# Kernel optimization log

Hardware: AMD Instinct MI355X
Metric: run time of the kernel (lower is better)

Reference implementation:

```python
import jax, jax.numpy as jnp
import numpy as np

B, LC, LT = 2, 1024, 1024
DS, DF = 2, 1
EOBS = 4                 # nn.Embed(2, 4)
D_IN = EOBS + DS + DF    # concat(obs, s, f)
EMB_H, D = 256, 64       # embed_obs_s_f = MLP([256, 64])
H, DH = 8, 8             # heads x head_dim = D
FFN_H = 128              # ffn = MLP([128, 64])
BIAS_H = 16              # DistanceBias hidden width
HEAD_H = 128             # head = MLP([128, 2])
NBLK = 6                 # num_blks (num_reps = 1)
EPS = 1e-6

def _ln(x, scale, bias):
    mu = jnp.mean(x, -1, keepdims=True)
    var = jnp.var(x, -1, keepdims=True)
    return (x - mu) * jax.lax.rsqrt(var + EPS) * scale + bias

def _mlp(x, w1, b1, w2, b2):
    return jax.nn.relu(x @ w1 + b1) @ w2 + b2

def _dist_bias(d, w1, b1, w2, b2):
    # d: [B, Lq, Lk] scalar distances -> per-head bias [B, H, Lq, Lk]
    h = jax.nn.relu(d[..., None] @ w1 + b1)
    return jnp.transpose(h @ w2 + b2, (0, 3, 1, 2))

def _mha(q_in, kv_in, wq, bq, wk, bk, wv, bv, wo, bo, bias):
    q = (q_in @ wq + bq).reshape(*q_in.shape[:-1], H, DH)
    k = (kv_in @ wk + bk).reshape(*kv_in.shape[:-1], H, DH)
    v = (kv_in @ wv + bv).reshape(*kv_in.shape[:-1], H, DH)
    scores = jnp.einsum('bqhd,bkhd->bhqk', q, k) / np.sqrt(DH).astype(np.float32) + bias
    a = jax.nn.softmax(scores, axis=-1)
    o = jnp.einsum('bhqk,bkhd->bqhd', a, v).reshape(*q_in.shape[:-1], D)
    return o @ wo + bo

def _forward(s_ctx, f_ctx, s_test, embed_obs_table, emb_w1, emb_b1, emb_w2, emb_b2,
             attn_wq, attn_bq, attn_wk, attn_bk, attn_wv, attn_bv, attn_wo, attn_bo,
             ffn_w1, ffn_b1, ffn_w2, ffn_b2, bias_w1, bias_b1, bias_w2, bias_b2,
             norm_scale, norm_bias, fnorm_scale, fnorm_bias,
             head_w1, head_b1, head_w2, head_b2):
    Bv, Lt = s_test.shape[0], s_test.shape[1]
    f_test = jnp.zeros((Bv, Lt, f_ctx.shape[-1]), f_ctx.dtype)
    obs = jnp.broadcast_to(embed_obs_table[1], (*f_ctx.shape[:-1], EOBS))
    unobs = jnp.broadcast_to(embed_obs_table[0], (Bv, Lt, EOBS))
    kvs = _mlp(jnp.concatenate([obs, s_ctx, f_ctx], -1), emb_w1, emb_b1, emb_w2, emb_b2)
    qvs = _mlp(jnp.concatenate([unobs, s_test, f_test], -1), emb_w1, emb_b1, emb_w2, emb_b2)
    # vmap(l2_dist_sq): pairwise squared L2 distances per batch element
    d_qk = jnp.sum((s_test[:, :, None, :] - s_ctx[:, None, :, :]) ** 2, -1)
    d_kk = jnp.sum((s_ctx[:, :, None, :] - s_ctx[:, None, :, :]) ** 2, -1)
    for i in range(NBLK):
        b_qk = _dist_bias(d_qk, bias_w1[i], bias_b1[i], bias_w2[i], bias_b2[i])
        b_kk = _dist_bias(d_kk, bias_w1[i], bias_b1[i], bias_w2[i], bias_b2[i])
        aw = (attn_wq[i], attn_bq[i], attn_wk[i], attn_bk[i], attn_wv[i], attn_bv[i], attn_wo[i], attn_bo[i])
        ns, nb = norm_scale[i], norm_bias[i]
        q_att = _ln(qvs + _mha(qvs, kvs, *aw, b_qk), ns, nb)
        k_att = _ln(kvs + _mha(kvs, kvs, *aw, b_kk), ns, nb)
        qvs = _ln(q_att + _mlp(q_att, ffn_w1[i], ffn_b1[i], ffn_w2[i], ffn_b2[i]), ns, nb)
        kvs = _ln(k_att + _mlp(k_att, ffn_w1[i], ffn_b1[i], ffn_w2[i], ffn_b2[i]), ns, nb)
    qvs = _ln(qvs, fnorm_scale, fnorm_bias)
    f_dist = _mlp(qvs, head_w1, head_b1, head_w2, head_b2)
    f_mu, f_log_var = jnp.split(f_dist, 2, axis=-1)
    f_std = jnp.exp(f_log_var / 2)  # min_std = 0.0
    return f_mu, f_std

def setup_inputs() -> dict:
    key = jax.random.key(0)
    ks = iter(jax.random.split(key, 40))
    r = lambda shp, s=0.05: jax.random.normal(next(ks), shp, jnp.float32) * s
    return dict(
        s_ctx=r((B, LC, DS), 1.0), f_ctx=r((B, LC, DF), 1.0), s_test=r((B, LT, DS), 1.0),
        embed_obs_table=r((2, EOBS)),
        emb_w1=r((D_IN, EMB_H)), emb_b1=jnp.zeros((EMB_H,)),
        emb_w2=r((EMB_H, D)), emb_b2=jnp.zeros((D,)),
        attn_wq=r((NBLK, D, D)), attn_bq=jnp.zeros((NBLK, D)),
        attn_wk=r((NBLK, D, D)), attn_bk=jnp.zeros((NBLK, D)),
        attn_wv=r((NBLK, D, D)), attn_bv=jnp.zeros((NBLK, D)),
        attn_wo=r((NBLK, D, D)), attn_bo=jnp.zeros((NBLK, D)),
        ffn_w1=r((NBLK, D, FFN_H)), ffn_b1=jnp.zeros((NBLK, FFN_H)),
        ffn_w2=r((NBLK, FFN_H, D)), ffn_b2=jnp.zeros((NBLK, D)),
        bias_w1=r((NBLK, 1, BIAS_H)), bias_b1=jnp.zeros((NBLK, BIAS_H)),
        bias_w2=r((NBLK, BIAS_H, H)), bias_b2=jnp.zeros((NBLK, H)),
        norm_scale=jnp.ones((NBLK, D)), norm_bias=jnp.zeros((NBLK, D)),
        fnorm_scale=jnp.ones((D,)), fnorm_bias=jnp.zeros((D,)),
        head_w1=r((D, HEAD_H)), head_b1=jnp.zeros((HEAD_H,)),
        head_w2=r((HEAD_H, 2)), head_b2=jnp.zeros((2,)),
    )

def reference(s_ctx, f_ctx, s_test, embed_obs_table, emb_w1, emb_b1, emb_w2, emb_b2,
              attn_wq, attn_bq, attn_wk, attn_bk, attn_wv, attn_bv, attn_wo, attn_bo,
              ffn_w1, ffn_b1, ffn_w2, ffn_b2, bias_w1, bias_b1, bias_w2, bias_b2,
              norm_scale, norm_bias, fnorm_scale, fnorm_bias,
              head_w1, head_b1, head_w2, head_b2):
    return _forward(s_ctx, f_ctx, s_test, embed_obs_table, emb_w1, emb_b1, emb_w2, emb_b2,
                    attn_wq, attn_bq, attn_wk, attn_bk, attn_wv, attn_bv, attn_wo, attn_bo,
                    ffn_w1, ffn_b1, ffn_w2, ffn_b2, bias_w1, bias_b1, bias_w2, bias_b2,
                    norm_scale, norm_bias, fnorm_scale, fnorm_bias,
                    head_w1, head_b1, head_w2, head_b2)
```

## Files before the change

### kernel.cpp

```cpp
#include <hip/hip_runtime.h>
#include <hip/hip_bf16.h>

typedef __hip_bfloat16 bf16;
typedef float v2f __attribute__((ext_vector_type(2)));

#define LEN 1024
#define N2 2048
#define SCALE_L2E 0.5100697918f

#define I_SCTX   0
#define I_FCTX   4096
#define I_STEST  6144
#define I_OBS    10240
#define I_EW1    10248
#define I_EB1    12040
#define I_EW2    12296
#define I_EB2    28680
#define I_WQ     28744
#define I_BQ     53320
#define I_WK     53704
#define I_BK     78280
#define I_WV     78664
#define I_BV     103240
#define I_WO     103624
#define I_BO     128200
#define I_FW1    128584
#define I_FB1    177736
#define I_FW2    178504
#define I_FB2    227656
#define I_BW1    228040
#define I_BB1    228136
#define I_BW2    228232
#define I_BB2    229000
#define I_NS     229048
#define I_NB     229432
#define I_FNS    229816
#define I_FNB    229880
#define I_HW1    229944
#define I_HB1    238136
#define I_HW2    238264
#define I_HB2    238520

#define OFF_FLAG 240000
#define OFF_PW   240256
#define OFF_QVS  262144
#define OFF_KVS  393216
#define OFF_Q1   524288
#define OFF_Q2   655360
#define OFF_KB   786432
#define OFF_VB   917504
#define OFF_PART 1048576

__constant__ int C_OFFS[33] = {
    0, 4096, 6144, 10240, 10248, 12040, 12296, 28680, 28744, 53320, 53704,
    78280, 78664, 103240, 103624, 128200, 128584, 177736, 178504, 227656,
    228040, 228136, 228232, 229000, 229048, 229432, 229816, 229880, 229944,
    238136, 238264, 238520, 238522 };

struct InPtrs { const void* p[32]; };

__global__ void k_flag(const void* ns_raw, float* ws) {
    if (threadIdx.x == 0) {
        unsigned u = *(const unsigned*)ns_raw;
        ((int*)(ws + OFF_FLAG))[0] = (u == 0x3F803F80u) ? 1 : 0;
    }
}

__global__ __launch_bounds__(256) void k_cvt(InPtrs ptrs, float* ws) {
    __shared__ int sflag;
    if (threadIdx.x == 0) sflag = ((const int*)(ws + OFF_FLAG))[0];
    __syncthreads();
    const int isbf = sflag;
    const int i = blockIdx.y;
    const int o0 = C_OFFS[i], n = C_OFFS[i + 1] - o0;
    const void* src = ptrs.p[i];
    for (int j = blockIdx.x * 256 + threadIdx.x; j < n; j += gridDim.x * 256) {
        float v = isbf ? __bfloat162float(((const bf16*)src)[j])
                       : ((const float*)src)[j];
        ws[o0 + j] = v;
    }
}

__global__ __launch_bounds__(256) void k_pw(float* ws) {
    const int L = blockIdx.x, t = threadIdx.x;
    __shared__ float w1s[16], b1s[16], bps[16];
    __shared__ int rnk[16];
    if (t < 16) {
        float w = ws[I_BW1 + L * 16 + t], b0 = ws[I_BB1 + L * 16 + t];
        w1s[t] = w; b1s[t] = b0;
        bps[t] = (w != 0.f) ? (-b0 / w) : 1e30f;
    }
    __syncthreads();
    if (t < 16) {
        float me = bps[t]; int r = 0;
        for (int j = 0; j < 16; ++j) {
            float o = bps[j];
            if (o < me || (o == me && j < t)) ++r;
        }
        rnk[t] = r;
    }
    __syncthreads();
    if (t < 16) ws[OFF_PW + L * 288 + 272 + rnk[t]] = bps[t];
    if (t < 136) {
        int s = t >> 3, h = t & 7;
        float slope = 0.f, inter = ws[I_BB2 + L * 8 + h];
        for (int j = 0; j < 16; ++j) {
            float w = w1s[j];
            bool act = (w > 0.f) ? (rnk[j] < s)
                     : (w < 0.f) ? (rnk[j] >= s)
                                 : (b1s[j] > 0.f);
            if (act) {
                float w2v = ws[I_BW2 + L * 128 + j * 8 + h];
                slope += w * w2v;
                inter += b1s[j] * w2v;
            }
        }
        const float LOG2E = 1.4426950408889634f;
        ws[OFF_PW + L * 288 + (s * 8 + h) * 2]     = slope * LOG2E;
        ws[OFF_PW + L * 288 + (s * 8 + h) * 2 + 1] = inter * LOG2E;
    }
}

__global__ __launch_bounds__(256) void k_embed(float* ws) {
    __shared__ float hbuf[256];
    __shared__ float red[256];
    int r = blockIdx.x, t = threadIdx.x;
    bool is_ctx = (r < N2);
    int rr = is_ctx ? r : r - N2;
    const float* ob = ws + I_OBS + (is_ctx ? 4 : 0);
    const float* s  = ws + (is_ctx ? I_SCTX : I_STEST);
    float in[7];
    in[0] = ob[0]; in[1] = ob[1]; in[2] = ob[2]; in[3] = ob[3];
    in[4] = s[rr * 2]; in[5] = s[rr * 2 + 1];
    in[6] = is_ctx ? ws[I_FCTX + rr] : 0.f;

    float acc = ws[I_EB1 + t];
#pragma unroll
    for (int i = 0; i < 7; ++i) acc += in[i] * ws[I_EW1 + i * 256 + t];
    hbuf[t] = fmaxf(acc, 0.f);
    __syncthreads();

    int d = t & 63, p = t >> 6;
    float a2 = 0.f;
#pragma unroll 8
    for (int j = p * 64; j < p * 64 + 64; ++j) a2 += hbuf[j] * ws[I_EW2 + j * 64 + d];
    red[t] = a2;
    __syncthreads();
    if (t < 64) {
        float o = red[t] + red[64 + t] + red[128 + t] + red[192 + t] + ws[I_EB2 + t];
        float* dst = ws + (is_ctx ? OFF_KVS : OFF_QVS);
        dst[rr * 64 + t] = o;
    }
}

__global__ __launch_bounds__(256) void k_qkv(int blk, float* ws) {
    __shared__ float xs[2][64];
    int r = blockIdx.x, t = threadIdx.x;
    if (t < 64)       xs[0][t] = ws[OFF_QVS + r * 64 + t];
    else if (t < 128) xs[1][t - 64] = ws[OFF_KVS + r * 64 + (t - 64)];
    __syncthreads();
    int o = t >> 6, d = t & 63;
    const float* x = (o == 0) ? xs[0] : xs[1];
    const float* W; const float* bb; float* dst;
    if (o <= 1)      { W = ws + I_WQ + blk * 4096; bb = ws + I_BQ + blk * 64; dst = ws + (o == 0 ? OFF_Q1 : OFF_Q2); }
    else if (o == 2) { W = ws + I_WK + blk * 4096; bb = ws + I_BK + blk * 64; dst = ws + OFF_KB; }
    else             { W = ws + I_WV + blk * 4096; bb = ws + I_BV + blk * 64; dst = ws + OFF_VB; }
    float acc = bb[d];
#pragma unroll 8
    for (int k = 0; k < 64; ++k) acc += x[k] * W[k * 64 + d];
    dst[r * 64 + d] = acc;
}

__global__ __launch_bounds__(256, 5) void k_attn(int blk, float* ws) {
    __shared__ float Ks[2176];
    __shared__ float Vs[2176];
    __shared__ v2f   Sds[544];
    __shared__ v2f   pw[136];

    const int t = threadIdx.x;
    const int qt = blockIdx.x, ks = blockIdx.y, z = blockIdx.z;
    const int b = z & 1, kind = z >> 1;
    const int q0 = qt * 16;
    const float* Qbuf = ws + (kind == 0 ? OFF_Q1 : OFF_Q2);
    const float* Kbuf = ws + OFF_KB;
    const float* Vbuf = ws + OFF_VB;
    const float* sq_src = ws + (kind == 0 ? I_STEST : I_SCTX);
    const float* sk_src = ws + I_SCTX;
    const float* pwg = ws + OFF_PW + blk * 288;

    float bp[16];
#pragma unroll
    for (int j = 0; j < 16; ++j) bp[j] = pwg[272 + j];

    if (t < 136) pw[t] = (v2f){ pwg[t * 2], pwg[t * 2 + 1] };

    const int q2 = t >> 4, h2 = (t >> 1) & 7, par = t & 1;
    const int tk = t & 15;

    v2f qf[4];
    {
        const float* qp = Qbuf + (b * LEN + q0 + q2) * 64 + h2 * 8;
        float4 qa = *(const float4*)qp;
        float4 qb = *(const float4*)(qp + 4);
        qf[0] = (v2f){qa.x, qa.y}; qf[1] = (v2f){qa.z, qa.w};
        qf[2] = (v2f){qb.x, qb.y}; qf[3] = (v2f){qb.z, qb.w};
    }
    float sqx, sqy;
    {
        const float* sp = sq_src + (b * LEN + q0 + q2) * 2;
        sqx = sp[0]; sqy = sp[1];
    }

    float m = -1e30f, lsum = 0.f;
    v2f oacc[4] = {};

    for (int kt = ks * 8; kt < ks * 8 + 8; ++kt) {
        __syncthreads();
        {
            int kr = t >> 3, j = (t & 7) * 8;
            const float* ksrc = Kbuf + (b * LEN + kt * 32 + kr) * 64 + j;
            const float* vsrc = Vbuf + (b * LEN + kt * 32 + kr) * 64 + j;
            *(float4*)&Ks[kr * 68 + j]     = *(const float4*)ksrc;
            *(float4*)&Ks[kr * 68 + j + 4] = *(const float4*)(ksrc + 4);
            *(float4*)&Vs[kr * 68 + j]     = *(const float4*)vsrc;
            *(float4*)&Vs[kr * 68 + j + 4] = *(const float4*)(vsrc + 4);
        }
        {
            float4 kc = *(const float4*)(sk_src + (b * LEN + kt * 32 + tk * 2) * 2);
            float dx0 = sqx - kc.x, dy0 = sqy - kc.y;
            float dx1 = sqx - kc.z, dy1 = sqy - kc.w;
            float d0 = dx0 * dx0 + dy0 * dy0;
            float d1 = dx1 * dx1 + dy1 * dy1;
            int s0 = 0, s1 = 0;
#pragma unroll
            for (int j = 0; j < 16; ++j) { s0 += (d0 > bp[j]); s1 += (d1 > bp[j]); }
            Sds[(tk * 2) * 17 + q2]     = (v2f){d0, (float)s0};
            Sds[(tk * 2 + 1) * 17 + q2] = (v2f){d1, (float)s1};
        }
        __syncthreads();

        float sv[16];
#pragma unroll
        for (int j = 0; j < 16; ++j) {
            int k = par + 2 * j;
            v2f dsv = Sds[k * 17 + q2];
            v2f pv_ = pw[(int)dsv.y * 8 + h2];
            const v2f* kf = (const v2f*)&Ks[k * 68 + h2 * 8];
            v2f acc = qf[0] * kf[0];
            acc += qf[1] * kf[1];
            acc += qf[2] * kf[2];
            acc += qf[3] * kf[3];
            sv[j] = (acc.x + acc.y) * SCALE_L2E + (pv_.x * dsv.x + pv_.y);
        }
        float tm = m;
#pragma unroll
        for (int j = 0; j < 16; ++j) tm = fmaxf(tm, sv[j]);
        float alpha = exp2f(m - tm);
        lsum *= alpha;
        v2f av = (v2f){alpha, alpha};
#pragma unroll
        for (int c = 0; c < 4; ++c) oacc[c] *= av;
#pragma unroll
        for (int j = 0; j < 16; ++j) {
            int k = par + 2 * j;
            float p = exp2f(sv[j] - tm);
            lsum += p;
            const v2f* vf = (const v2f*)&Vs[k * 68 + h2 * 8];
            v2f pp = (v2f){p, p};
            oacc[0] += pp * vf[0];
            oacc[1] += pp * vf[1];
            oacc[2] += pp * vf[2];
            oacc[3] += pp * vf[3];
        }
        m = tm;
    }

    {
        float mo = __shfl_xor(m, 1);
        float Mx = fmaxf(m, mo);
        float a0 = exp2f(m - Mx), a1 = exp2f(mo - Mx);
        float lo = __shfl_xor(lsum, 1);
        float Lt = lsum * a0 + lo * a1;
        float ov[8];
#pragma unroll
        for (int c = 0; c < 4; ++c) {
            v2f x = oacc[c];
            ov[2 * c]     = x.x * a0 + __shfl_xor(x.x, 1) * a1;
            ov[2 * c + 1] = x.y * a0 + __shfl_xor(x.y, 1) * a1;
        }
        if (par == 0) {
            float* p = ws + OFF_PART + (z * LEN + q0 + q2) * 384 + (h2 * 4 + ks) * 12;
            *(float4*)(p)     = make_float4(ov[0], ov[1], ov[2], ov[3]);
            *(float4*)(p + 4) = make_float4(ov[4], ov[5], ov[6], ov[7]);
            *(float4*)(p + 8) = make_float4(Mx, Lt, 0.f, 0.f);
        }
    }
}

__global__ __launch_bounds__(128) void k_fuse(int blk, float* ws) {
    __shared__ float raw[384];
    __shared__ float xo[64];
    __shared__ float xs[64];
    __shared__ float hs[128];
    __shared__ float xn[64];
    const int r = blockIdx.x, kind = blockIdx.y, t = threadIdx.x;
    const int b = r >> 10, row = r & 1023;
    const int z = kind * 2 + b;
    float* io = ws + (kind == 0 ? OFF_QVS : OFF_KVS);

    const float* pbase = ws + OFF_PART + (z * LEN + row) * 384;
    if (t < 96) *(float4*)&raw[t * 4] = *(const float4*)&pbase[t * 4];
    __syncthreads();

    if (t < 64) {
        int h = t >> 3, d = t & 7;
        float M = -1e30f;
#pragma unroll
        for (int k2 = 0; k2 < 4; ++k2) M = fmaxf(M, raw[(h * 4 + k2) * 12 + 8]);
        float L = 0.f, o = 0.f;
#pragma unroll
        for (int k2 = 0; k2 < 4; ++k2) {
            float e = exp2f(raw[(h * 4 + k2) * 12 + 8] - M);
            L += raw[(h * 4 + k2) * 12 + 9] * e;
            o += raw[(h * 4 + k2) * 12 + d] * e;
        }
        xo[t] = o / L;
    }
    __syncthreads();

    if (t < 64) {
        const float* Wo = ws + I_WO + blk * 4096;
        float acc = ws[I_BO + blk * 64 + t];
#pragma unroll 8
        for (int j = 0; j < 64; ++j) acc += xo[j] * Wo[j * 64 + t];
        acc += io[r * 64 + t];
        float s = acc, ss2 = acc * acc;
#pragma unroll
        for (int off = 1; off < 64; off <<= 1) { s += __shfl_xor(s, off); ss2 += __shfl_xor(ss2, off); }
        float mu_ = s * (1.f / 64.f);
        float var_ = ss2 * (1.f / 64.f) - mu_ * mu_;
        float rs_ = rsqrtf(fmaxf(var_, 0.f) + 1e-6f);
        xs[t] = (acc - mu_) * rs_ * ws[I_NS + blk * 64 + t] + ws[I_NB + blk * 64 + t];
    }
    __syncthreads();

    {
        const float* W1 = ws + I_FW1 + blk * 8192;
        float acc = ws[I_FB1 + blk * 128 + t];
#pragma unroll 8
        for (int k = 0; k < 64; ++k) acc += xs[k] * W1[k * 128 + t];
        hs[t] = fmaxf(acc, 0.f);
    }
    __syncthreads();

    if (t < 64) {
        const float* W2 = ws + I_FW2 + blk * 8192;
        float a2 = ws[I_FB2 + blk * 64 + t];
#pragma unroll 8
        for (int k = 0; k < 128; ++k) a2 += hs[k] * W2[k * 64 + t];
        a2 += xs[t];
        float s = a2, ss2 = a2 * a2;
#pragma unroll
        for (int off = 1; off < 64; off <<= 1) { s += __shfl_xor(s, off); ss2 += __shfl_xor(ss2, off); }
        float mu_ = s * (1.f / 64.f);
        float var_ = ss2 * (1.f / 64.f) - mu_ * mu_;
        float rs_ = rsqrtf(fmaxf(var_, 0.f) + 1e-6f);
        float outv = (a2 - mu_) * rs_ * ws[I_NS + blk * 64 + t] + ws[I_NB + blk * 64 + t];
        io[r * 64 + t] = outv;
        xn[t] = outv;
    }
    __syncthreads();

    if (blk < 5) {
        const int nb_ = blk + 1;
        if (kind == 0) {
            if (t < 64) {
                const float* W = ws + I_WQ + nb_ * 4096;
                float acc = ws[I_BQ + nb_ * 64 + t];
#pragma unroll 8
                for (int k = 0; k < 64; ++k) acc += xn[k] * W[k * 64 + t];
                ws[OFF_Q1 + r * 64 + t] = acc;
            }
        } else {
            {
                int pj = t >> 6, d = t & 63;
                const float* W  = ws + (pj == 0 ? I_WQ : I_WK) + nb_ * 4096;
                const float* bb = ws + (pj == 0 ? I_BQ : I_BK) + nb_ * 64;
                float acc = bb[d];
#pragma unroll 8
                for (int k = 0; k < 64; ++k) acc += xn[k] * W[k * 64 + d];
                float* dst = ws + (pj == 0 ? OFF_Q2 : OFF_KB);
                dst[r * 64 + d] = acc;
            }
            if (t < 64) {
                const float* W = ws + I_WV + nb_ * 4096;
                float acc = ws[I_BV + nb_ * 64 + t];
#pragma unroll 8
                for (int k = 0; k < 64; ++k) acc += xn[k] * W[k * 64 + t];
                ws[OFF_VB + r * 64 + t] = acc;
            }
        }
    }
}

__global__ __launch_bounds__(128) void k_head(float* ws, void* out_raw) {
    __shared__ float xl[64];
    __shared__ float hl[128];
    __shared__ int sflag;
    int r = blockIdx.x, t = threadIdx.x;
    if (t == 0) sflag = ((const int*)(ws + OFF_FLAG))[0];
    if (t < 64) {
        float v = ws[OFF_QVS + r * 64 + t];
        float s = v, ss2 = v * v;
#pragma unroll
        for (int off = 1; off < 64; off <<= 1) { s += __shfl_xor(s, off); ss2 += __shfl_xor(ss2, off); }
        float mu_ = s * (1.f / 64.f);
        float var_ = ss2 * (1.f / 64.f) - mu_ * mu_;
        float rs_ = rsqrtf(fmaxf(var_, 0.f) + 1e-6f);
        xl[t] = (v - mu_) * rs_ * ws[I_FNS + t] + ws[I_FNB + t];
    }
    __syncthreads();
    float acc = ws[I_HB1 + t];
#pragma unroll 8
    for (int k = 0; k < 64; ++k) acc += xl[k] * ws[I_HW1 + k * 128 + t];
    hl[t] = fmaxf(acc, 0.f);
    __syncthreads();
    if (t < 2) {
        float a = ws[I_HB2 + t];
        for (int j = 0; j < 128; ++j) a += hl[j] * ws[I_HW2 + j * 2 + t];
        float v = (t == 0) ? a : __expf(a * 0.5f);
        int idx = (t == 0) ? r : (N2 + r);
        if (sflag) ((bf16*)out_raw)[idx] = __float2bfloat16(v);
        else       ((float*)out_raw)[idx] = v;
    }
}

extern "C" void kernel_launch(void* const* d_in, const int* in_sizes, int n_in,
                              void* d_out, int out_size, void* d_ws, size_t ws_size,
                              hipStream_t stream) {
    float* ws = (float*)d_ws;

    InPtrs ptrs;
    for (int i = 0; i < 32; ++i) ptrs.p[i] = d_in[i];

    k_flag<<<1, 64, 0, stream>>>(d_in[24], ws);
    k_cvt<<<dim3(8, 32), 256, 0, stream>>>(ptrs, ws);
    k_pw<<<6, 256, 0, stream>>>(ws);
    k_embed<<<4096, 256, 0, stream>>>(ws);
    k_qkv<<<2048, 256, 0, stream>>>(0, ws);
    for (int i = 0; i < 6; ++i) {
        k_attn<<<dim3(64, 4, 4), 256, 0, stream>>>(i, ws);
        k_fuse<<<dim3(2048, 2), 128, 0, stream>>>(i, ws);
    }
    k_head<<<2048, 128, 0, stream>>>(ws, d_out);
}
```

Before: 528.6 us.

## Split attention keys finer, pack partials as bf16, batch fuse rows, merge head

The attention kernel now splits the key range into 8 chunks instead of 4, allows higher occupancy, and packs the bias bucket index into the low bits of the distance. It also writes normalised partial outputs as bf16 pairs plus a log-sum-exp, which cuts partial-buffer traffic. The fuse kernel handles 8 rows per 256-thread block with vectorised weight loads, merges the Q/K/V projections into one loop, and absorbs the final head MLP. The separate flag and head kernels are removed. Storing partials in bf16 and truncating distance mantissa bits add some rounding error.

```diff
diff --git a/kernel.cpp b/kernel.cpp
--- a/kernel.cpp
+++ b/kernel.cpp
@@ -41,7 +41,6 @@
 #define I_HW2    238264
 #define I_HB2    238520
 
-#define OFF_FLAG 240000
 #define OFF_PW   240256
 #define OFF_QVS  262144
 #define OFF_KVS  393216
@@ -59,18 +58,21 @@
 
 struct InPtrs { const void* p[32]; };
 
-__global__ void k_flag(const void* ns_raw, float* ws) {
-    if (threadIdx.x == 0) {
-        unsigned u = *(const unsigned*)ns_raw;
-        ((int*)(ws + OFF_FLAG))[0] = (u == 0x3F803F80u) ? 1 : 0;
-    }
+__device__ __forceinline__ float pack2(float a, float b) {
+    __hip_bfloat16 ha = __float2bfloat16(a), hb = __float2bfloat16(b);
+    unsigned ua = *(unsigned short*)&ha, ub = *(unsigned short*)&hb;
+    return __uint_as_float(ua | (ub << 16));
+}
+__device__ __forceinline__ float unlo(float f) {
+    return __uint_as_float(__float_as_uint(f) << 16);
+}
+__device__ __forceinline__ float unhi(float f) {
+    return __uint_as_float(__float_as_uint(f) & 0xffff0000u);
 }
 
 __global__ __launch_bounds__(256) void k_cvt(InPtrs ptrs, float* ws) {
-    __shared__ int sflag;
-    if (threadIdx.x == 0) sflag = ((const int*)(ws + OFF_FLAG))[0];
-    __syncthreads();
-    const int isbf = sflag;
+    const unsigned u0 = *(const unsigned*)ptrs.p[24];
+    const int isbf = (u0 == 0x3F803F80u);
     const int i = blockIdx.y;
     const int o0 = C_OFFS[i], n = C_OFFS[i + 1] - o0;
     const void* src = ptrs.p[i];
@@ -171,10 +173,10 @@
     dst[r * 64 + d] = acc;
 }
 
-__global__ __launch_bounds__(256, 5) void k_attn(int blk, float* ws) {
+__global__ __launch_bounds__(256, 8) void k_attn(int blk, float* ws) {
     __shared__ float Ks[2176];
-    __shared__ float Vs[2176];
-    __shared__ v2f   Sds[544];
+    __shared__ float Vs[2112];
+    __shared__ float Sds[544];
     __shared__ v2f   pw[136];
 
     const int t = threadIdx.x;
@@ -214,16 +216,20 @@
     float m = -1e30f, lsum = 0.f;
     v2f oacc[4] = {};
 
-    for (int kt = ks * 8; kt < ks * 8 + 8; ++kt) {
+    for (int kt = ks * 4; kt < ks * 4 + 4; ++kt) {
         __syncthreads();
         {
             int kr = t >> 3, j = (t & 7) * 8;
             const float* ksrc = Kbuf + (b * LEN + kt * 32 + kr) * 64 + j;
             const float* vsrc = Vbuf + (b * LEN + kt * 32 + kr) * 64 + j;
-            *(float4*)&Ks[kr * 68 + j]     = *(const float4*)ksrc;
-            *(float4*)&Ks[kr * 68 + j + 4] = *(const float4*)(ksrc + 4);
-            *(float4*)&Vs[kr * 68 + j]     = *(const float4*)vsrc;
-            *(float4*)&Vs[kr * 68 + j + 4] = *(const float4*)(vsrc + 4);
+            float4 ka = *(const float4*)ksrc, kb = *(const float4*)(ksrc + 4);
+            *(float4*)&Ks[kr * 68 + j]     = ka;
+            *(float4*)&Ks[kr * 68 + j + 4] = kb;
+            float4 va = *(const float4*)vsrc, vb = *(const float4*)(vsrc + 4);
+            *(v2f*)&Vs[kr * 66 + j]     = (v2f){va.x, va.y};
+            *(v2f*)&Vs[kr * 66 + j + 2] = (v2f){va.z, va.w};
+            *(v2f*)&Vs[kr * 66 + j + 4] = (v2f){vb.x, vb.y};
+            *(v2f*)&Vs[kr * 66 + j + 6] = (v2f){vb.z, vb.w};
         }
         {
             float4 kc = *(const float4*)(sk_src + (b * LEN + kt * 32 + tk * 2) * 2);
@@ -234,8 +240,8 @@
             int s0 = 0, s1 = 0;
 #pragma unroll
             for (int j = 0; j < 16; ++j) { s0 += (d0 > bp[j]); s1 += (d1 > bp[j]); }
-            Sds[(tk * 2) * 17 + q2]     = (v2f){d0, (float)s0};
-            Sds[(tk * 2 + 1) * 17 + q2] = (v2f){d1, (float)s1};
+            Sds[(tk * 2) * 17 + q2]     = __uint_as_float((__float_as_uint(d0) & ~31u) | s0);
+            Sds[(tk * 2 + 1) * 17 + q2] = __uint_as_float((__float_as_uint(d1) & ~31u) | s1);
         }
         __syncthreads();
 
@@ -243,14 +249,15 @@
 #pragma unroll
         for (int j = 0; j < 16; ++j) {
             int k = par + 2 * j;
-            v2f dsv = Sds[k * 17 + q2];
-            v2f pv_ = pw[(int)dsv.y * 8 + h2];
+            unsigned u = __float_as_uint(Sds[k * 17 + q2]);
+            float dv = __uint_as_float(u & ~31u);
+            v2f pv_ = pw[(u & 31u) * 8 + h2];
             const v2f* kf = (const v2f*)&Ks[k * 68 + h2 * 8];
             v2f acc = qf[0] * kf[0];
             acc += qf[1] * kf[1];
             acc += qf[2] * kf[2];
             acc += qf[3] * kf[3];
-            sv[j] = (acc.x + acc.y) * SCALE_L2E + (pv_.x * dsv.x + pv_.y);
+            sv[j] = (acc.x + acc.y) * SCALE_L2E + (pv_.x * dv + pv_.y);
         }
         float tm = m;
 #pragma unroll
@@ -265,7 +272,7 @@
             int k = par + 2 * j;
             float p = exp2f(sv[j] - tm);
             lsum += p;
-            const v2f* vf = (const v2f*)&Vs[k * 68 + h2 * 8];
+            const v2f* vf = (const v2f*)&Vs[k * 66 + h2 * 8];
             v2f pp = (v2f){p, p};
             oacc[0] += pp * vf[0];
             oacc[1] += pp * vf[1];
@@ -289,149 +296,202 @@
             ov[2 * c + 1] = x.y * a0 + __shfl_xor(x.y, 1) * a1;
         }
         if (par == 0) {
-            float* p = ws + OFF_PART + (z * LEN + q0 + q2) * 384 + (h2 * 4 + ks) * 12;
-            *(float4*)(p)     = make_float4(ov[0], ov[1], ov[2], ov[3]);
-            *(float4*)(p + 4) = make_float4(ov[4], ov[5], ov[6], ov[7]);
-            *(float4*)(p + 8) = make_float4(Mx, Lt, 0.f, 0.f);
-        }
-    }
-}
-
-__global__ __launch_bounds__(128) void k_fuse(int blk, float* ws) {
-    __shared__ float raw[384];
-    __shared__ float xo[64];
-    __shared__ float xs[64];
-    __shared__ float hs[128];
-    __shared__ float xn[64];
-    const int r = blockIdx.x, kind = blockIdx.y, t = threadIdx.x;
-    const int b = r >> 10, row = r & 1023;
-    const int z = kind * 2 + b;
+            float inv = 1.f / Lt;
+            float lse = Mx + log2f(Lt);
+            float* p = ws + OFF_PART + ((z * LEN + q0 + q2) * 8 + h2) * 48 + ks * 6;
+            *(v2f*)(p)     = (v2f){ pack2(ov[0] * inv, ov[1] * inv), pack2(ov[2] * inv, ov[3] * inv) };
+            *(v2f*)(p + 2) = (v2f){ pack2(ov[4] * inv, ov[5] * inv), pack2(ov[6] * inv, ov[7] * inv) };
+            *(v2f*)(p + 4) = (v2f){ lse, 0.f };
+        }
+    }
+}
+
+__global__ __launch_bounds__(256) void k_fuse(int blk, float* ws, const void* ns_raw, void* out_raw) {
+    __shared__ float xo[8 * 68];
+    __shared__ float xsm[8 * 68];
+    __shared__ float hs[8 * 132];
+    __shared__ float xn[8 * 68];
+    const int t = threadIdx.x;
+    const int kind = blockIdx.y;
+    const int r0 = blockIdx.x * 8;
     float* io = ws + (kind == 0 ? OFF_QVS : OFF_KVS);
 
-    const float* pbase = ws + OFF_PART + (z * LEN + row) * 384;
-    if (t < 96) *(float4*)&raw[t * 4] = *(const float4*)&pbase[t * 4];
-    __syncthreads();
-
-    if (t < 64) {
-        int h = t >> 3, d = t & 7;
-        float M = -1e30f;
-#pragma unroll
-        for (int k2 = 0; k2 < 4; ++k2) M = fmaxf(M, raw[(h * 4 + k2) * 12 + 8]);
-        float L = 0.f, o = 0.f;
-#pragma unroll
-        for (int k2 = 0; k2 < 4; ++k2) {
-            float e = exp2f(raw[(h * 4 + k2) * 12 + 8] - M);
-            L += raw[(h * 4 + k2) * 12 + 9] * e;
-            o += raw[(h * 4 + k2) * 12 + d] * e;
-        }
-        xo[t] = o / L;
-    }
-    __syncthreads();
-
-    if (t < 64) {
+    {
+        int r = t >> 5, h = (t >> 2) & 7, q = t & 3;
+        int rg = r0 + r, b = rg >> 10, row = rg & 1023, z = kind * 2 + b;
+        const float* e0 = ws + OFF_PART + ((z * LEN + row) * 8 + h) * 48 + q * 6;
+        v2f a0 = *(const v2f*)e0, a1 = *(const v2f*)(e0 + 2), a2 = *(const v2f*)(e0 + 4);
+        v2f c0 = *(const v2f*)(e0 + 24), c1 = *(const v2f*)(e0 + 26), c2 = *(const v2f*)(e0 + 28);
+        float M = fmaxf(a2.x, c2.x);
+        M = fmaxf(M, __shfl_xor(M, 1));
+        M = fmaxf(M, __shfl_xor(M, 2));
+        float wA = exp2f(a2.x - M), wB = exp2f(c2.x - M);
+        float den = wA + wB;
+        float num[8];
+        num[0] = wA * unlo(a0.x) + wB * unlo(c0.x);
+        num[1] = wA * unhi(a0.x) + wB * unhi(c0.x);
+        num[2] = wA * unlo(a0.y) + wB * unlo(c0.y);
+        num[3] = wA * unhi(a0.y) + wB * unhi(c0.y);
+        num[4] = wA * unlo(a1.x) + wB * unlo(c1.x);
+        num[5] = wA * unhi(a1.x) + wB * unhi(c1.x);
+        num[6] = wA * unlo(a1.y) + wB * unlo(c1.y);
+        num[7] = wA * unhi(a1.y) + wB * unhi(c1.y);
+        den += __shfl_xor(den, 1); den += __shfl_xor(den, 2);
+#pragma unroll
+        for (int d_ = 0; d_ < 8; ++d_) {
+            num[d_] += __shfl_xor(num[d_], 1);
+            num[d_] += __shfl_xor(num[d_], 2);
+        }
+        float invd = 1.f / den;
+        xo[r * 68 + h * 8 + 2 * q]     = num[2 * q] * invd;
+        xo[r * 68 + h * 8 + 2 * q + 1] = num[2 * q + 1] * invd;
+    }
+    __syncthreads();
+
+    const int r = t >> 5, dd = (t & 31) * 2;
+    const int rg = r0 + r;
+    float xs0, xs1;
+
+    {
         const float* Wo = ws + I_WO + blk * 4096;
-        float acc = ws[I_BO + blk * 64 + t];
+        v2f acc = *(const v2f*)(ws + I_BO + blk * 64 + dd);
 #pragma unroll 8
-        for (int j = 0; j < 64; ++j) acc += xo[j] * Wo[j * 64 + t];
-        acc += io[r * 64 + t];
-        float s = acc, ss2 = acc * acc;
-#pragma unroll
-        for (int off = 1; off < 64; off <<= 1) { s += __shfl_xor(s, off); ss2 += __shfl_xor(ss2, off); }
-        float mu_ = s * (1.f / 64.f);
-        float var_ = ss2 * (1.f / 64.f) - mu_ * mu_;
-        float rs_ = rsqrtf(fmaxf(var_, 0.f) + 1e-6f);
-        xs[t] = (acc - mu_) * rs_ * ws[I_NS + blk * 64 + t] + ws[I_NB + blk * 64 + t];
-    }
-    __syncthreads();
-
-    {
+        for (int k = 0; k < 64; ++k) {
+            float xv = xo[r * 68 + k];
+            v2f w = *(const v2f*)(Wo + k * 64 + dd);
+            acc.x += xv * w.x; acc.y += xv * w.y;
+        }
+        v2f rv = *(const v2f*)(io + rg * 64 + dd);
+        acc.x += rv.x; acc.y += rv.y;
+        float s = acc.x + acc.y, s2 = acc.x * acc.x + acc.y * acc.y;
+#pragma unroll
+        for (int off = 1; off < 32; off <<= 1) { s += __shfl_xor(s, off); s2 += __shfl_xor(s2, off); }
+        float mu = s * (1.f / 64.f);
+        float var = s2 * (1.f / 64.f) - mu * mu;
+        float rs = rsqrtf(fmaxf(var, 0.f) + 1e-6f);
+        v2f nsv = *(const v2f*)(ws + I_NS + blk * 64 + dd);
+        v2f nbv = *(const v2f*)(ws + I_NB + blk * 64 + dd);
+        xs0 = (acc.x - mu) * rs * nsv.x + nbv.x;
+        xs1 = (acc.y - mu) * rs * nsv.y + nbv.y;
+        *(v2f*)&xsm[r * 68 + dd] = (v2f){xs0, xs1};
+    }
+    __syncthreads();
+
+    {
+        int rc = t >> 5, c4 = (t & 31) * 4;
         const float* W1 = ws + I_FW1 + blk * 8192;
-        float acc = ws[I_FB1 + blk * 128 + t];
+        float4 acc = *(const float4*)(ws + I_FB1 + blk * 128 + c4);
+#pragma unroll 4
+        for (int k = 0; k < 64; ++k) {
+            float xv = xsm[rc * 68 + k];
+            float4 w = *(const float4*)(W1 + k * 128 + c4);
+            acc.x += xv * w.x; acc.y += xv * w.y; acc.z += xv * w.z; acc.w += xv * w.w;
+        }
+        acc.x = fmaxf(acc.x, 0.f); acc.y = fmaxf(acc.y, 0.f);
+        acc.z = fmaxf(acc.z, 0.f); acc.w = fmaxf(acc.w, 0.f);
+        *(float4*)&hs[rc * 132 + c4] = acc;
+    }
+    __syncthreads();
+
+    float v0, v1;
+    {
+        const float* W2 = ws + I_FW2 + blk * 8192;
+        v2f acc = *(const v2f*)(ws + I_FB2 + blk * 64 + dd);
 #pragma unroll 8
-        for (int k = 0; k < 64; ++k) acc += xs[k] * W1[k * 128 + t];
-        hs[t] = fmaxf(acc, 0.f);
-    }
-    __syncthreads();
-
-    if (t < 64) {
-        const float* W2 = ws + I_FW2 + blk * 8192;
-        float a2 = ws[I_FB2 + blk * 64 + t];
-#pragma unroll 8
-        for (int k = 0; k < 128; ++k) a2 += hs[k] * W2[k * 64 + t];
-        a2 += xs[t];
-        float s = a2, ss2 = a2 * a2;
-#pragma unroll
-        for (int off = 1; off < 64; off <<= 1) { s += __shfl_xor(s, off); ss2 += __shfl_xor(ss2, off); }
-        float mu_ = s * (1.f / 64.f);
-        float var_ = ss2 * (1.f / 64.f) - mu_ * mu_;
-        float rs_ = rsqrtf(fmaxf(var_, 0.f) + 1e-6f);
-        float outv = (a2 - mu_) * rs_ * ws[I_NS + blk * 64 + t] + ws[I_NB + blk * 64 + t];
-        io[r * 64 + t] = outv;
-        xn[t] = outv;
+        for (int k = 0; k < 128; ++k) {
+            float hv = hs[r * 132 + k];
+            v2f w = *(const v2f*)(W2 + k * 64 + dd);
+            acc.x += hv * w.x; acc.y += hv * w.y;
+        }
+        acc.x += xs0; acc.y += xs1;
+        float s = acc.x + acc.y, s2 = acc.x * acc.x + acc.y * acc.y;
+#pragma unroll
+        for (int off = 1; off < 32; off <<= 1) { s += __shfl_xor(s, off); s2 += __shfl_xor(s2, off); }
+        float mu = s * (1.f / 64.f);
+        float var = s2 * (1.f / 64.f) - mu * mu;
+        float rs = rsqrtf(fmaxf(var, 0.f) + 1e-6f);
+        v2f nsv = *(const v2f*)(ws + I_NS + blk * 64 + dd);
+        v2f nbv = *(const v2f*)(ws + I_NB + blk * 64 + dd);
+        v0 = (acc.x - mu) * rs * nsv.x + nbv.x;
+        v1 = (acc.y - mu) * rs * nsv.y + nbv.y;
+        *(v2f*)(io + rg * 64 + dd) = (v2f){v0, v1};
+        *(v2f*)&xn[r * 68 + dd] = (v2f){v0, v1};
     }
     __syncthreads();
 
     if (blk < 5) {
         const int nb_ = blk + 1;
         if (kind == 0) {
-            if (t < 64) {
-                const float* W = ws + I_WQ + nb_ * 4096;
-                float acc = ws[I_BQ + nb_ * 64 + t];
+            const float* WQ = ws + I_WQ + nb_ * 4096;
+            v2f acc = *(const v2f*)(ws + I_BQ + nb_ * 64 + dd);
 #pragma unroll 8
-                for (int k = 0; k < 64; ++k) acc += xn[k] * W[k * 64 + t];
-                ws[OFF_Q1 + r * 64 + t] = acc;
+            for (int k = 0; k < 64; ++k) {
+                float xv = xn[r * 68 + k];
+                v2f w = *(const v2f*)(WQ + k * 64 + dd);
+                acc.x += xv * w.x; acc.y += xv * w.y;
             }
+            *(v2f*)(ws + OFF_Q1 + rg * 64 + dd) = acc;
         } else {
-            {
-                int pj = t >> 6, d = t & 63;
-                const float* W  = ws + (pj == 0 ? I_WQ : I_WK) + nb_ * 4096;
-                const float* bb = ws + (pj == 0 ? I_BQ : I_BK) + nb_ * 64;
-                float acc = bb[d];
-#pragma unroll 8
-                for (int k = 0; k < 64; ++k) acc += xn[k] * W[k * 64 + d];
-                float* dst = ws + (pj == 0 ? OFF_Q2 : OFF_KB);
-                dst[r * 64 + d] = acc;
+            const float* WQ = ws + I_WQ + nb_ * 4096;
+            const float* WK = ws + I_WK + nb_ * 4096;
+            const float* WV = ws + I_WV + nb_ * 4096;
+            v2f aq = *(const v2f*)(ws + I_BQ + nb_ * 64 + dd);
+            v2f ak = *(const v2f*)(ws + I_BK + nb_ * 64 + dd);
+            v2f av = *(const v2f*)(ws + I_BV + nb_ * 64 + dd);
+#pragma unroll 4
+            for (int k = 0; k < 64; ++k) {
+                float xv = xn[r * 68 + k];
+                v2f wq = *(const v2f*)(WQ + k * 64 + dd);
+                v2f wk = *(const v2f*)(WK + k * 64 + dd);
+                v2f wv = *(const v2f*)(WV + k * 64 + dd);
+                aq.x += xv * wq.x; aq.y += xv * wq.y;
+                ak.x += xv * wk.x; ak.y += xv * wk.y;
+                av.x += xv * wv.x; av.y += xv * wv.y;
             }
-            if (t < 64) {
-                const float* W = ws + I_WV + nb_ * 4096;
-                float acc = ws[I_BV + nb_ * 64 + t];
-#pragma unroll 8
-                for (int k = 0; k < 64; ++k) acc += xn[k] * W[k * 64 + t];
-                ws[OFF_VB + r * 64 + t] = acc;
+            *(v2f*)(ws + OFF_Q2 + rg * 64 + dd) = aq;
+            *(v2f*)(ws + OFF_KB + rg * 64 + dd) = ak;
+            *(v2f*)(ws + OFF_VB + rg * 64 + dd) = av;
+        }
+    } else if (kind == 0) {
+        {
+            float s = v0 + v1, s2 = v0 * v0 + v1 * v1;
+#pragma unroll
+            for (int off = 1; off < 32; off <<= 1) { s += __shfl_xor(s, off); s2 += __shfl_xor(s2, off); }
+            float mu = s * (1.f / 64.f);
+            float var = s2 * (1.f / 64.f) - mu * mu;
+            float rs = rsqrtf(fmaxf(var, 0.f) + 1e-6f);
+            v2f fns = *(const v2f*)(ws + I_FNS + dd);
+            v2f fnb = *(const v2f*)(ws + I_FNB + dd);
+            *(v2f*)&xsm[r * 68 + dd] = (v2f){ (v0 - mu) * rs * fns.x + fnb.x,
+                                              (v1 - mu) * rs * fns.y + fnb.y };
+        }
+        __syncthreads();
+        {
+            int rc = t >> 5, c4 = (t & 31) * 4;
+            const float* W1 = ws + I_HW1;
+            float4 acc = *(const float4*)(ws + I_HB1 + c4);
+#pragma unroll 4
+            for (int k = 0; k < 64; ++k) {
+                float xv = xsm[rc * 68 + k];
+                float4 w = *(const float4*)(W1 + k * 128 + c4);
+                acc.x += xv * w.x; acc.y += xv * w.y; acc.z += xv * w.z; acc.w += xv * w.w;
             }
-        }
-    }
-}
-
-__global__ __launch_bounds__(128) void k_head(float* ws, void* out_raw) {
-    __shared__ float xl[64];
-    __shared__ float hl[128];
-    __shared__ int sflag;
-    int r = blockIdx.x, t = threadIdx.x;
-    if (t == 0) sflag = ((const int*)(ws + OFF_FLAG))[0];
-    if (t < 64) {
-        float v = ws[OFF_QVS + r * 64 + t];
-        float s = v, ss2 = v * v;
-#pragma unroll
-        for (int off = 1; off < 64; off <<= 1) { s += __shfl_xor(s, off); ss2 += __shfl_xor(ss2, off); }
-        float mu_ = s * (1.f / 64.f);
-        float var_ = ss2 * (1.f / 64.f) - mu_ * mu_;
-        float rs_ = rsqrtf(fmaxf(var_, 0.f) + 1e-6f);
-        xl[t] = (v - mu_) * rs_ * ws[I_FNS + t] + ws[I_FNB + t];
-    }
-    __syncthreads();
-    float acc = ws[I_HB1 + t];
-#pragma unroll 8
-    for (int k = 0; k < 64; ++k) acc += xl[k] * ws[I_HW1 + k * 128 + t];
-    hl[t] = fmaxf(acc, 0.f);
-    __syncthreads();
-    if (t < 2) {
-        float a = ws[I_HB2 + t];
-        for (int j = 0; j < 128; ++j) a += hl[j] * ws[I_HW2 + j * 2 + t];
-        float v = (t == 0) ? a : __expf(a * 0.5f);
-        int idx = (t == 0) ? r : (N2 + r);
-        if (sflag) ((bf16*)out_raw)[idx] = __float2bfloat16(v);
-        else       ((float*)out_raw)[idx] = v;
+            acc.x = fmaxf(acc.x, 0.f); acc.y = fmaxf(acc.y, 0.f);
+            acc.z = fmaxf(acc.z, 0.f); acc.w = fmaxf(acc.w, 0.f);
+            *(float4*)&hs[rc * 132 + c4] = acc;
+        }
+        __syncthreads();
+        if (t < 16) {
+            int rr = t >> 1, c = t & 1;
+            float a = ws[I_HB2 + c];
+            for (int k = 0; k < 128; ++k) a += hs[rr * 132 + k] * ws[I_HW2 + k * 2 + c];
+            float v = c ? exp2f(a * 0.7213475204444817f) : a;
+            int rgg = r0 + rr;
+            int idx = c ? (N2 + rgg) : rgg;
+            unsigned u0 = *(const unsigned*)ns_raw;
+            if (u0 == 0x3F803F80u) ((bf16*)out_raw)[idx] = __float2bfloat16(v);
+            else                   ((float*)out_raw)[idx] = v;
+        }
     }
 }
 
@@ -443,14 +503,12 @@
     InPtrs ptrs;
     for (int i = 0; i < 32; ++i) ptrs.p[i] = d_in[i];
 
-    k_flag<<<1, 64, 0, stream>>>(d_in[24], ws);
     k_cvt<<<dim3(8, 32), 256, 0, stream>>>(ptrs, ws);
     k_pw<<<6, 256, 0, stream>>>(ws);
     k_embed<<<4096, 256, 0, stream>>>(ws);
     k_qkv<<<2048, 256, 0, stream>>>(0, ws);
     for (int i = 0; i < 6; ++i) {
-        k_attn<<<dim3(64, 4, 4), 256, 0, stream>>>(i, ws);
-        k_fuse<<<dim3(2048, 2), 128, 0, stream>>>(i, ws);
-    }
-    k_head<<<2048, 128, 0, stream>>>(ws, d_out);
-}
+        k_attn<<<dim3(64, 8, 4), 256, 0, stream>>>(i, ws);
+        k_fuse<<<dim3(256, 2), 256, 0, stream>>>(i, ws, d_in[24], d_out);
+    }
+}
```

Result: slower. 652.7 us (+23.5%).
